# Kernel optimization log

Measured on AMD Instinct MI355X. Metric: run time of the kernel, lower is better.

The kernel has to match this reference:

```python
import jax, jax.numpy as jnp
import numpy as np

B, N, F = 32, 64, 128   # batch, nodes, input features (F == hidden_dim)
E = N * (N - 1)         # fully-connected directed edges = 4032
H, D = 4, 64            # heads, out_dim per head
ALPHA = 0.2             # leaky relu slope


def setup_inputs() -> dict:
    key = jax.random.key(0)
    ks = jax.random.split(key, 16)
    v_self = jax.random.normal(ks[0], (B, N, F), dtype=jnp.float32)
    # fully-connected one-hot sender/receiver matrices [E, N], broadcast to [B, E, N]
    pairs = np.array([(i, j) for i in range(N) for j in range(N) if i != j])
    send = np.zeros((E, N), np.float32); send[np.arange(E), pairs[:, 0]] = 1.0
    rec = np.zeros((E, N), np.float32); rec[np.arange(E), pairs[:, 1]] = 1.0
    rel_send = jnp.broadcast_to(jnp.asarray(send), (B, E, N))
    rel_rec = jnp.broadcast_to(jnp.asarray(rec), (B, E, N))
    s = 0.05
    return {
        "v_self": v_self,
        "rel_rec": rel_rec,
        "rel_send": rel_send,
        "W_proj": jax.random.normal(ks[1], (H * D, F), dtype=jnp.float32) * s,
        "a_fwd": jax.random.normal(ks[2], (H, D), dtype=jnp.float32) * s,
        "a_bwd": jax.random.normal(ks[3], (H, D), dtype=jnp.float32) * s,
        "We1": jax.random.normal(ks[4], (D, 2 * D), dtype=jnp.float32) * s,
        "be1": jnp.zeros((D,), jnp.float32),
        "We2": jax.random.normal(ks[5], (D, D), dtype=jnp.float32) * s,
        "be2": jnp.zeros((D,), jnp.float32),
        "Wv1": jax.random.normal(ks[6], (F, D), dtype=jnp.float32) * s,
        "bv1": jnp.zeros((F,), jnp.float32),
        "Wv2": jax.random.normal(ks[7], (F, F), dtype=jnp.float32) * s,
        "bv2": jnp.zeros((F,), jnp.float32),
        "Wv3": jax.random.normal(ks[8], (D, F), dtype=jnp.float32) * s,
        "bv3": jnp.zeros((D,), jnp.float32),
    }


def _leaky(x):
    return jnp.where(x >= 0, x, ALPHA * x)


def reference(v_self, rel_rec, rel_send, W_proj, a_fwd, a_bwd,
              We1, be1, We2, be2, Wv1, bv1, Wv2, bv2, Wv3, bv3):
    # project: [B,N,F] -> [B,N,H,D]
    v_proj = (v_self @ W_proj.T).reshape(B, N, H, D)
    # gather to edges via one-hot adjacency (v_src==h_src, v_tgt==h_tgt in original)
    h_src = jnp.einsum('ben,bnhd->behd', rel_send, v_proj)
    h_tgt = jnp.einsum('ben,bnhd->behd', rel_rec, v_proj)
    attn_ij = _leaky(jnp.einsum('behd,hd->beh', h_src, a_fwd)) / 500.0
    attn_ji = _leaky(jnp.einsum('behd,hd->beh', h_tgt, a_bwd)) / 500.0
    attn_max = jnp.maximum(attn_ij, attn_ji)
    # NOTE: original applies exp twice (exp of exp); reproduced faithfully
    e_ij = jnp.exp(jnp.exp(attn_ij - attn_max))
    e_ji = jnp.exp(jnp.exp(attn_ji - attn_max))
    alpha_sum = e_ij + e_ji
    alpha_ij = e_ij / alpha_sum   # [B,E,H]
    alpha_ji = e_ji / alpha_sum
    edge_input = jnp.concatenate(
        [alpha_ij[..., None] * h_src, alpha_ji[..., None] * h_tgt], axis=-1)  # [B,E,H,2D]
    # f_CG_e: Linear(2D->D), ReLU, Linear(D->D) on last dim
    e_cg = jax.nn.relu(edge_input @ We1.T + be1) @ We2.T + be2
    edge_weighted = e_cg * alpha_ij[..., None]                               # [B,E,H,D]
    # scatter back to nodes
    v_social = jnp.einsum('behd,ben->bnhd', edge_weighted, rel_rec)          # [B,N,H,D]
    # f_CG_v: Linear(D->F), ReLU, Linear(F->F), ReLU, Linear(F->D)
    x = jax.nn.relu(v_social @ Wv1.T + bv1)
    x = jax.nn.relu(x @ Wv2.T + bv2)
    x = x @ Wv3.T + bv3
    v_out = x.reshape(B, N, H * D)  # concat_heads=True
    return (v_out, alpha_ij)
```

## Files before the change

### kernel.cpp

```cpp
#include <hip/hip_runtime.h>

#define B_ 32
#define N_ 64
#define F_ 128
#define E_ 4032
#define H_ 4
#define D_ 64

typedef __bf16 bf16x8 __attribute__((ext_vector_type(8)));
typedef __bf16 bf16x4 __attribute__((ext_vector_type(4)));
typedef float  f32x4  __attribute__((ext_vector_type(4)));


static __device__ inline bf16x8 ld_cvt8(const float* __restrict__ p) {
    float4 w0 = *(const float4*)p, w1 = *(const float4*)(p + 4);
    bf16x8 b;
    b[0]=(__bf16)w0.x; b[1]=(__bf16)w0.y; b[2]=(__bf16)w0.z; b[3]=(__bf16)w0.w;
    b[4]=(__bf16)w1.x; b[5]=(__bf16)w1.y; b[6]=(__bf16)w1.z; b[7]=(__bf16)w1.w;
    return b;
}

__global__ __launch_bounds__(64) void k_proj(
    const float* __restrict__ v_self, const float* __restrict__ W_proj,
    const float* __restrict__ We1,
    const float* __restrict__ a_fwd, const float* __restrict__ a_bwd,
    const float* __restrict__ Wv1, const float* __restrict__ We2,
    const float* __restrict__ be2, const float* __restrict__ Wv2,
    const float* __restrict__ Wv3,
    float* __restrict__ s_fwd, float* __restrict__ s_bwd,
    __bf16* __restrict__ u_src, __bf16* __restrict__ u_tgt,
    __bf16* __restrict__ M1bf, float* __restrict__ wb,
    __bf16* __restrict__ Wv2bf, __bf16* __restrict__ Wv3bf)
{
    const int t = threadIdx.x;
    const int blk = blockIdx.x;

    if (blk >= 512) {
        const int f = blk - 512;
        const int k = t;
        const int pid = f * 64 + k;
        float acc = 0.f;
        for (int dd = 0; dd < 64; ++dd)
            acc += Wv1[f * 64 + dd] * We2[dd * 64 + k];
        M1bf[pid] = (__bf16)acc;
        float p = Wv1[f * 64 + k] * be2[k];
#pragma unroll
        for (int m = 1; m < 64; m <<= 1) p += __shfl_xor(p, m);
        if (k == 0) wb[f] = p;
        Wv2bf[pid]        = (__bf16)Wv2[pid];
        Wv2bf[pid + 8192] = (__bf16)Wv2[pid + 8192];
        Wv3bf[pid]        = (__bf16)Wv3[pid];
        return;
    }

    const int tile = blk >> 2, w = blk & 3;
    const int node0 = tile * 16;
    const int q = t >> 4, lr = t & 15;

    __shared__ __bf16 P_lds[16 * 72];

    f32x4 acc[4] = {};
#pragma unroll
    for (int ks = 0; ks < 4; ++ks) {
        bf16x8 a = ld_cvt8(v_self + (size_t)(node0 + lr) * 128 + ks * 32 + q * 8);
#pragma unroll
        for (int ct = 0; ct < 4; ++ct) {
            bf16x8 bb = ld_cvt8(W_proj + (size_t)(w * 64 + ct * 16 + lr) * 128 + ks * 32 + q * 8);
            acc[ct] = __builtin_amdgcn_mfma_f32_16x16x32_bf16(a, bb, acc[ct], 0, 0, 0);
        }
    }

    {
        float pf[4] = {0,0,0,0}, pb[4] = {0,0,0,0};
#pragma unroll
        for (int ct = 0; ct < 4; ++ct) {
            float af = a_fwd[w * 64 + ct * 16 + lr];
            float ab = a_bwd[w * 64 + ct * 16 + lr];
#pragma unroll
            for (int r = 0; r < 4; ++r) { pf[r] += acc[ct][r] * af; pb[r] += acc[ct][r] * ab; }
        }
#pragma unroll
        for (int m = 1; m < 16; m <<= 1) {
#pragma unroll
            for (int r = 0; r < 4; ++r) { pf[r] += __shfl_xor(pf[r], m); pb[r] += __shfl_xor(pb[r], m); }
        }
        if (lr == 0) {
#pragma unroll
            for (int r = 0; r < 4; ++r) {
                float x = pf[r]; x = (x >= 0.f ? x : 0.2f * x) * 0.002f;
                float y = pb[r]; y = (y >= 0.f ? y : 0.2f * y) * 0.002f;
                s_fwd[(node0 + q * 4 + r) * 4 + w] = x;
                s_bwd[(node0 + q * 4 + r) * 4 + w] = y;
            }
        }
    }

#pragma unroll
    for (int ct = 0; ct < 4; ++ct)
#pragma unroll
        for (int r = 0; r < 4; ++r)
            P_lds[(q * 4 + r) * 72 + ct * 16 + lr] = (__bf16)acc[ct][r];
    __syncthreads();

    f32x4 us[4] = {}, ut[4] = {};
#pragma unroll
    for (int ks = 0; ks < 2; ++ks) {
        bf16x8 a = *(const bf16x8*)&P_lds[lr * 72 + ks * 32 + q * 8];
#pragma unroll
        for (int ct = 0; ct < 4; ++ct) {
            bf16x8 bs = ld_cvt8(We1 + (size_t)(ct * 16 + lr) * 128 + ks * 32 + q * 8);
            us[ct] = __builtin_amdgcn_mfma_f32_16x16x32_bf16(a, bs, us[ct], 0, 0, 0);
            bf16x8 bt = ld_cvt8(We1 + (size_t)(ct * 16 + lr) * 128 + 64 + ks * 32 + q * 8);
            ut[ct] = __builtin_amdgcn_mfma_f32_16x16x32_bf16(a, bt, ut[ct], 0, 0, 0);
        }
    }
#pragma unroll
    for (int ct = 0; ct < 4; ++ct)
#pragma unroll
        for (int r = 0; r < 4; ++r) {
            size_t row = (size_t)(node0 + q * 4 + r) * 4 + w;
            u_src[row * 64 + ct * 16 + lr] = (__bf16)us[ct][r];
            u_tgt[row * 64 + ct * 16 + lr] = (__bf16)ut[ct][r];
        }
}

__global__ __launch_bounds__(256) void k_fused(
    const float* __restrict__ s_fwd, const float* __restrict__ s_bwd,
    const __bf16* __restrict__ u_src, const __bf16* __restrict__ u_tgt,
    const float* __restrict__ be1,
    const __bf16* __restrict__ M1bf, const float* __restrict__ wb,
    const float* __restrict__ bv1,
    const __bf16* __restrict__ Wv2bf, const float* __restrict__ bv2,
    const __bf16* __restrict__ Wv3bf, const float* __restrict__ bv3,
    float* __restrict__ v_out, float* __restrict__ out_alpha)
{
    const int t = threadIdx.x;
    const int h = t >> 6, d = t & 63;
    const int b = blockIdx.x >> 4, quad = blockIdx.x & 15;
    const int j0 = quad * 4;

    __shared__ float  ut_l[4][4][64];
    __shared__ float  aij_l[4][64][4];
    __shared__ float  suma_l[16];
    __shared__ __bf16 g_l[16 * 72];
    __shared__ __bf16 X1[16 * 136];
    __shared__ __bf16 X2[16 * 136];

    {
        int idx = t * 4;
        bf16x4 v = *(const bf16x4*)(u_tgt + (size_t)(b * 64 + j0) * 256 + idx);
        int j = idx >> 8, col = idx & 255;
        f32x4 f;
#pragma unroll
        for (int z = 0; z < 4; ++z) f[z] = (float)v[z];
        *(f32x4*)&ut_l[j][col >> 6][col & 63] = f;
    }

    {
        const int i = d;
        float sfi = s_fwd[(b * 64 + i) * 4 + h];
        float areg[4];
#pragma unroll
        for (int jl = 0; jl < 4; ++jl) {
            float sbj = s_bwd[(b * 64 + j0 + jl) * 4 + h];
            float m = fmaxf(sfi, sbj);
            float eij = __expf(__expf(sfi - m));
            float eji = __expf(__expf(sbj - m));
            float aij = eij / (eij + eji);
            if (i == j0 + jl) aij = 0.f;
            areg[jl] = aij;
        }
        f32x4 a4 = {areg[0], areg[1], areg[2], areg[3]};
        *(f32x4*)&aij_l[h][i][0] = a4;
#pragma unroll
        for (int jl = 0; jl < 4; ++jl) {
            float sa = areg[jl];
#pragma unroll
            for (int m2 = 1; m2 < 64; m2 <<= 1) sa += __shfl_xor(sa, m2);
            if (i == 0) suma_l[jl * 4 + h] = sa;
        }
    }
    if (t < 252) {
        const int jj = t >> 2, h2 = t & 3;
#pragma unroll
        for (int s = 0; s < 4; ++s) {
            int i2 = j0 + s;
            int j2 = jj + (jj >= i2 ? 1 : 0);
            float sfi = s_fwd[(b * 64 + i2) * 4 + h2];
            float sbj = s_bwd[(b * 64 + j2) * 4 + h2];
            float m = fmaxf(sfi, sbj);
            float eij = __expf(__expf(sfi - m));
            float eji = __expf(__expf(sbj - m));
            out_alpha[((size_t)b * E_ + i2 * 63 + jj) * 4 + h2] = eij / (eij + eji);
        }
    }
    __syncthreads();

    {
        const float be1d = be1[d];
        float utv[4], utb[4];
#pragma unroll
        for (int jl = 0; jl < 4; ++jl) { utv[jl] = ut_l[jl][h][d]; utb[jl] = utv[jl] + be1d; }
        float gacc[4] = {};
        const __bf16* usp = u_src + ((size_t)(b * 64) * 4 + h) * 64 + d;
#pragma unroll 4
        for (int i = 0; i < 64; ++i) {
            float usv = (float)usp[i * 256];
            f32x4 a4 = *(const f32x4*)&aij_l[h][i][0];
#pragma unroll
            for (int jl = 0; jl < 4; ++jl) {
                float a = a4[jl];
                float hp = fmaf(a, usv - utv[jl], utb[jl]);
                gacc[jl] = fmaf(a, fmaxf(hp, 0.f), gacc[jl]);
            }
        }
#pragma unroll
        for (int jl = 0; jl < 4; ++jl)
            g_l[(jl * 4 + h) * 72 + d] = (__bf16)gacc[jl];
    }
    __syncthreads();

    const int w = h;
    const int q = d >> 4, lr = d & 15;

    f32x4 acc1[2] = {};
#pragma unroll
    for (int ks = 0; ks < 2; ++ks) {
        bf16x8 a = *(const bf16x8*)&g_l[lr * 72 + ks * 32 + q * 8];
#pragma unroll
        for (int c = 0; c < 2; ++c) {
            int ct = w * 2 + c;
            bf16x8 bb = *(const bf16x8*)(M1bf + (size_t)(ct * 16 + lr) * 64 + ks * 32 + q * 8);
            acc1[c] = __builtin_amdgcn_mfma_f32_16x16x32_bf16(a, bb, acc1[c], 0, 0, 0);
        }
    }
    float sml[4];
#pragma unroll
    for (int r = 0; r < 4; ++r) sml[r] = suma_l[q * 4 + r];
#pragma unroll
    for (int c = 0; c < 2; ++c) {
        int f = (w * 2 + c) * 16 + lr;
        float wbf = wb[f], b1 = bv1[f];
#pragma unroll
        for (int r = 0; r < 4; ++r) {
            float xv = acc1[c][r] + sml[r] * wbf + b1;
            X1[(q * 4 + r) * 136 + f] = (__bf16)fmaxf(xv, 0.f);
        }
    }
    __syncthreads();

    f32x4 acc2[2] = {};
#pragma unroll
    for (int ks = 0; ks < 4; ++ks) {
        bf16x8 a = *(const bf16x8*)&X1[lr * 136 + ks * 32 + q * 8];
#pragma unroll
        for (int c = 0; c < 2; ++c) {
            int ct = w * 2 + c;
            bf16x8 bb = *(const bf16x8*)(Wv2bf + (size_t)(ct * 16 + lr) * 128 + ks * 32 + q * 8);
            acc2[c] = __builtin_amdgcn_mfma_f32_16x16x32_bf16(a, bb, acc2[c], 0, 0, 0);
        }
    }
#pragma unroll
    for (int c = 0; c < 2; ++c) {
        int f = (w * 2 + c) * 16 + lr;
        float b2 = bv2[f];
#pragma unroll
        for (int r = 0; r < 4; ++r) {
            float xv = acc2[c][r] + b2;
            X2[(q * 4 + r) * 136 + f] = (__bf16)fmaxf(xv, 0.f);
        }
    }
    __syncthreads();

    f32x4 acc3 = {};
#pragma unroll
    for (int ks = 0; ks < 4; ++ks) {
        bf16x8 a = *(const bf16x8*)&X2[lr * 136 + ks * 32 + q * 8];
        bf16x8 bb = *(const bf16x8*)(Wv3bf + (size_t)(w * 16 + lr) * 128 + ks * 32 + q * 8);
        acc3 = __builtin_amdgcn_mfma_f32_16x16x32_bf16(a, bb, acc3, 0, 0, 0);
    }
    {
        int dd = w * 16 + lr;
        float b3 = bv3[dd];
        size_t rows_base = (size_t)(b * 64 + j0) * 4;
#pragma unroll
        for (int r = 0; r < 4; ++r)
            v_out[(rows_base + q * 4 + r) * 64 + dd] = acc3[r] + b3;
    }
}

extern "C" void kernel_launch(void* const* d_in, const int* in_sizes, int n_in,
                              void* d_out, int out_size, void* d_ws, size_t ws_size,
                              hipStream_t stream) {
    (void)in_sizes; (void)n_in; (void)out_size; (void)ws_size;
    const float* v_self = (const float*)d_in[0];
    const float* W_proj = (const float*)d_in[3];
    const float* a_fwd  = (const float*)d_in[4];
    const float* a_bwd  = (const float*)d_in[5];
    const float* We1    = (const float*)d_in[6];
    const float* be1    = (const float*)d_in[7];
    const float* We2    = (const float*)d_in[8];
    const float* be2    = (const float*)d_in[9];
    const float* Wv1    = (const float*)d_in[10];
    const float* bv1    = (const float*)d_in[11];
    const float* Wv2    = (const float*)d_in[12];
    const float* bv2    = (const float*)d_in[13];
    const float* Wv3    = (const float*)d_in[14];
    const float* bv3    = (const float*)d_in[15];

    float* ws = (float*)d_ws;
    float*  s_fwd = ws;
    float*  s_bwd = ws + 8192;
    float*  wb    = ws + 24576;
    __bf16* M1bf  = (__bf16*)(ws + 24704);
    __bf16* Wv2bf = (__bf16*)(ws + 28800);
    __bf16* Wv3bf = (__bf16*)(ws + 36992);
    __bf16* u_src = (__bf16*)(ws + 61568);
    __bf16* u_tgt = (__bf16*)(ws + 323712);

    float* v_out = (float*)d_out;
    float* alpha = v_out + (size_t)B_ * N_ * H_ * D_;

    hipLaunchKernelGGL(k_proj, dim3(512 + 128), dim3(64), 0, stream,
                       v_self, W_proj, We1, a_fwd, a_bwd, Wv1, We2, be2, Wv2, Wv3,
                       s_fwd, s_bwd, u_src, u_tgt, M1bf, wb, Wv2bf, Wv3bf);
    hipLaunchKernelGGL(k_fused, dim3(B_ * N_ / 4), dim3(256), 0, stream,
                       s_fwd, s_bwd, u_src, u_tgt, be1, M1bf, wb, bv1,
                       Wv2bf, bv2, Wv3bf, bv3, v_out, alpha);
}
```

Measured before the change: 29.11 us.

## Split projection K-loop and We1 halves across waves in 256-thread blocks

k_proj now runs 256-thread blocks holding two projection tiles. The two waves of each tile split the W_proj K-loop, and their partial accumulators are summed through LDS. In the second stage each wave computes either the u_src or the u_tgt half of the We1 product. The weight-prep branch is repacked to 256 threads per block, and the k_fused edge loop unroll goes from 4 to 8. The aim is shorter per-wave serial MFMA chains and fewer launched blocks, at the cost of an extra LDS reduction and barrier.

```diff
diff --git a/kernel.cpp b/kernel.cpp
--- a/kernel.cpp
+++ b/kernel.cpp
@@ -20,7 +20,7 @@
     return b;
 }
 
-__global__ __launch_bounds__(64) void k_proj(
+__global__ __launch_bounds__(256) void k_proj(
     const float* __restrict__ v_self, const float* __restrict__ W_proj,
     const float* __restrict__ We1,
     const float* __restrict__ a_fwd, const float* __restrict__ a_bwd,
@@ -35,11 +35,11 @@
     const int t = threadIdx.x;
     const int blk = blockIdx.x;
 
-    if (blk >= 512) {
-        const int f = blk - 512;
-        const int k = t;
-        const int pid = f * 64 + k;
+    if (blk >= 256) {
+        const int pid = (blk - 256) * 256 + t;
+        const int f = pid >> 6, k = pid & 63;
         float acc = 0.f;
+#pragma unroll 8
         for (int dd = 0; dd < 64; ++dd)
             acc += Wv1[f * 64 + dd] * We2[dd * 64 + k];
         M1bf[pid] = (__bf16)acc;
@@ -53,15 +53,20 @@
         return;
     }
 
-    const int tile = blk >> 2, w = blk & 3;
+    const int u = t >> 7;
+    const int wsub = (t >> 6) & 1;
+    const int l = t & 63, q = l >> 4, lr = l & 15;
+    const int gu = blk * 2 + u;
+    const int tile = gu >> 2, w = gu & 3;
     const int node0 = tile * 16;
-    const int q = t >> 4, lr = t & 15;
-
-    __shared__ __bf16 P_lds[16 * 72];
+
+    __shared__ float  accp[2][16][68];
+    __shared__ __bf16 P_lds[2][16 * 72];
 
     f32x4 acc[4] = {};
 #pragma unroll
-    for (int ks = 0; ks < 4; ++ks) {
+    for (int kk = 0; kk < 2; ++kk) {
+        int ks = wsub * 2 + kk;
         bf16x8 a = ld_cvt8(v_self + (size_t)(node0 + lr) * 128 + ks * 32 + q * 8);
 #pragma unroll
         for (int ct = 0; ct < 4; ++ct) {
@@ -69,15 +74,28 @@
             acc[ct] = __builtin_amdgcn_mfma_f32_16x16x32_bf16(a, bb, acc[ct], 0, 0, 0);
         }
     }
-
-    {
+    if (wsub == 1) {
+#pragma unroll
+        for (int ct = 0; ct < 4; ++ct)
+#pragma unroll
+            for (int r = 0; r < 4; ++r)
+                accp[u][q * 4 + r][ct * 16 + lr] = acc[ct][r];
+    }
+    __syncthreads();
+
+    if (wsub == 0) {
         float pf[4] = {0,0,0,0}, pb[4] = {0,0,0,0};
 #pragma unroll
         for (int ct = 0; ct < 4; ++ct) {
             float af = a_fwd[w * 64 + ct * 16 + lr];
             float ab = a_bwd[w * 64 + ct * 16 + lr];
 #pragma unroll
-            for (int r = 0; r < 4; ++r) { pf[r] += acc[ct][r] * af; pb[r] += acc[ct][r] * ab; }
+            for (int r = 0; r < 4; ++r) {
+                float full = acc[ct][r] + accp[u][q * 4 + r][ct * 16 + lr];
+                acc[ct][r] = full;
+                pf[r] += full * af;
+                pb[r] += full * ab;
+            }
         }
 #pragma unroll
         for (int m = 1; m < 16; m <<= 1) {
@@ -93,34 +111,32 @@
                 s_bwd[(node0 + q * 4 + r) * 4 + w] = y;
             }
         }
-    }
-
-#pragma unroll
-    for (int ct = 0; ct < 4; ++ct)
-#pragma unroll
-        for (int r = 0; r < 4; ++r)
-            P_lds[(q * 4 + r) * 72 + ct * 16 + lr] = (__bf16)acc[ct][r];
-    __syncthreads();
-
-    f32x4 us[4] = {}, ut[4] = {};
+#pragma unroll
+        for (int ct = 0; ct < 4; ++ct)
+#pragma unroll
+            for (int r = 0; r < 4; ++r)
+                P_lds[u][(q * 4 + r) * 72 + ct * 16 + lr] = (__bf16)acc[ct][r];
+    }
+    __syncthreads();
+
+    const int mm = wsub;
+    f32x4 uacc[4] = {};
 #pragma unroll
     for (int ks = 0; ks < 2; ++ks) {
-        bf16x8 a = *(const bf16x8*)&P_lds[lr * 72 + ks * 32 + q * 8];
+        bf16x8 a = *(const bf16x8*)&P_lds[u][lr * 72 + ks * 32 + q * 8];
 #pragma unroll
         for (int ct = 0; ct < 4; ++ct) {
-            bf16x8 bs = ld_cvt8(We1 + (size_t)(ct * 16 + lr) * 128 + ks * 32 + q * 8);
-            us[ct] = __builtin_amdgcn_mfma_f32_16x16x32_bf16(a, bs, us[ct], 0, 0, 0);
-            bf16x8 bt = ld_cvt8(We1 + (size_t)(ct * 16 + lr) * 128 + 64 + ks * 32 + q * 8);
-            ut[ct] = __builtin_amdgcn_mfma_f32_16x16x32_bf16(a, bt, ut[ct], 0, 0, 0);
-        }
-    }
+            bf16x8 bb = ld_cvt8(We1 + (size_t)(ct * 16 + lr) * 128 + mm * 64 + ks * 32 + q * 8);
+            uacc[ct] = __builtin_amdgcn_mfma_f32_16x16x32_bf16(a, bb, uacc[ct], 0, 0, 0);
+        }
+    }
+    __bf16* up = (mm == 0) ? u_src : u_tgt;
 #pragma unroll
     for (int ct = 0; ct < 4; ++ct)
 #pragma unroll
         for (int r = 0; r < 4; ++r) {
             size_t row = (size_t)(node0 + q * 4 + r) * 4 + w;
-            u_src[row * 64 + ct * 16 + lr] = (__bf16)us[ct][r];
-            u_tgt[row * 64 + ct * 16 + lr] = (__bf16)ut[ct][r];
+            up[row * 64 + ct * 16 + lr] = (__bf16)uacc[ct][r];
         }
 }
 
@@ -203,7 +219,7 @@
         for (int jl = 0; jl < 4; ++jl) { utv[jl] = ut_l[jl][h][d]; utb[jl] = utv[jl] + be1d; }
         float gacc[4] = {};
         const __bf16* usp = u_src + ((size_t)(b * 64) * 4 + h) * 64 + d;
-#pragma unroll 4
+#pragma unroll 8
         for (int i = 0; i < 64; ++i) {
             float usv = (float)usp[i * 256];
             f32x4 a4 = *(const f32x4*)&aij_l[h][i][0];
@@ -321,7 +337,7 @@
     float* v_out = (float*)d_out;
     float* alpha = v_out + (size_t)B_ * N_ * H_ * D_;
 
-    hipLaunchKernelGGL(k_proj, dim3(512 + 128), dim3(64), 0, stream,
+    hipLaunchKernelGGL(k_proj, dim3(256 + 32), dim3(256), 0, stream,
                        v_self, W_proj, We1, a_fwd, a_bwd, Wv1, We2, be2, Wv2, Wv3,
                        s_fwd, s_bwd, u_src, u_tgt, M1bf, wb, Wv2bf, Wv3bf);
     hipLaunchKernelGGL(k_fused, dim3(B_ * N_ / 4), dim3(256), 0, stream,
```

New measurement: 26.14 us. 10.2% less time.

## Fuse projection and We1 GEMMs into main kernel, keep per-batch intermediates in LDS

Applied to the files above, without the earlier changes.

The projection GEMM, attention scores and u_src/u_tgt products move from the prep kernel into the main kernel. Each block recomputes the whole batch's projection (64 nodes × 4 heads) and keeps u_src, s_fwd and s_bwd in shared memory, so the global round trip for these intermediates goes away. The prep kernel now only converts inputs and weights to bf16. The cost is that each batch's projection is computed redundantly by all 16 blocks of that batch, and the main kernel uses more LDS and registers, which can lower occupancy.

```diff
diff --git a/kernel.cpp b/kernel.cpp
--- a/kernel.cpp
+++ b/kernel.cpp
@@ -8,125 +8,58 @@
 #define D_ 64
 
 typedef __bf16 bf16x8 __attribute__((ext_vector_type(8)));
-typedef __bf16 bf16x4 __attribute__((ext_vector_type(4)));
 typedef float  f32x4  __attribute__((ext_vector_type(4)));
 
 
-static __device__ inline bf16x8 ld_cvt8(const float* __restrict__ p) {
-    float4 w0 = *(const float4*)p, w1 = *(const float4*)(p + 4);
-    bf16x8 b;
-    b[0]=(__bf16)w0.x; b[1]=(__bf16)w0.y; b[2]=(__bf16)w0.z; b[3]=(__bf16)w0.w;
-    b[4]=(__bf16)w1.x; b[5]=(__bf16)w1.y; b[6]=(__bf16)w1.z; b[7]=(__bf16)w1.w;
-    return b;
-}
-
-__global__ __launch_bounds__(64) void k_proj(
+#define MFMA(a, b, c) __builtin_amdgcn_mfma_f32_16x16x32_bf16(a, b, c, 0, 0, 0)
+
+__global__ __launch_bounds__(256) void k_prep(
     const float* __restrict__ v_self, const float* __restrict__ W_proj,
-    const float* __restrict__ We1,
-    const float* __restrict__ a_fwd, const float* __restrict__ a_bwd,
-    const float* __restrict__ Wv1, const float* __restrict__ We2,
-    const float* __restrict__ be2, const float* __restrict__ Wv2,
-    const float* __restrict__ Wv3,
-    float* __restrict__ s_fwd, float* __restrict__ s_bwd,
-    __bf16* __restrict__ u_src, __bf16* __restrict__ u_tgt,
-    __bf16* __restrict__ M1bf, float* __restrict__ wb,
-    __bf16* __restrict__ Wv2bf, __bf16* __restrict__ Wv3bf)
+    const float* __restrict__ We1, const float* __restrict__ Wv1,
+    const float* __restrict__ We2, const float* __restrict__ be2,
+    const float* __restrict__ Wv2, const float* __restrict__ Wv3,
+    __bf16* __restrict__ vbf, __bf16* __restrict__ Wpbf,
+    __bf16* __restrict__ We1bf, __bf16* __restrict__ M1bf,
+    float* __restrict__ wb, __bf16* __restrict__ Wv2bf,
+    __bf16* __restrict__ Wv3bf)
 {
     const int t = threadIdx.x;
     const int blk = blockIdx.x;
 
-    if (blk >= 512) {
-        const int f = blk - 512;
-        const int k = t;
-        const int pid = f * 64 + k;
-        float acc = 0.f;
-        for (int dd = 0; dd < 64; ++dd)
-            acc += Wv1[f * 64 + dd] * We2[dd * 64 + k];
-        M1bf[pid] = (__bf16)acc;
-        float p = Wv1[f * 64 + k] * be2[k];
-#pragma unroll
-        for (int m = 1; m < 64; m <<= 1) p += __shfl_xor(p, m);
-        if (k == 0) wb[f] = p;
-        Wv2bf[pid]        = (__bf16)Wv2[pid];
-        Wv2bf[pid + 8192] = (__bf16)Wv2[pid + 8192];
-        Wv3bf[pid]        = (__bf16)Wv3[pid];
+    if (blk < 128) {
+        int idx = blk * 2048 + t * 8;
+        float4 v0 = *(const float4*)(v_self + idx);
+        float4 v1 = *(const float4*)(v_self + idx + 4);
+        bf16x8 b;
+        b[0]=(__bf16)v0.x; b[1]=(__bf16)v0.y; b[2]=(__bf16)v0.z; b[3]=(__bf16)v0.w;
+        b[4]=(__bf16)v1.x; b[5]=(__bf16)v1.y; b[6]=(__bf16)v1.z; b[7]=(__bf16)v1.w;
+        *(bf16x8*)(vbf + idx) = b;
         return;
     }
 
-    const int tile = blk >> 2, w = blk & 3;
-    const int node0 = tile * 16;
-    const int q = t >> 4, lr = t & 15;
-
-    __shared__ __bf16 P_lds[16 * 72];
-
-    f32x4 acc[4] = {};
-#pragma unroll
-    for (int ks = 0; ks < 4; ++ks) {
-        bf16x8 a = ld_cvt8(v_self + (size_t)(node0 + lr) * 128 + ks * 32 + q * 8);
-#pragma unroll
-        for (int ct = 0; ct < 4; ++ct) {
-            bf16x8 bb = ld_cvt8(W_proj + (size_t)(w * 64 + ct * 16 + lr) * 128 + ks * 32 + q * 8);
-            acc[ct] = __builtin_amdgcn_mfma_f32_16x16x32_bf16(a, bb, acc[ct], 0, 0, 0);
-        }
-    }
-
-    {
-        float pf[4] = {0,0,0,0}, pb[4] = {0,0,0,0};
-#pragma unroll
-        for (int ct = 0; ct < 4; ++ct) {
-            float af = a_fwd[w * 64 + ct * 16 + lr];
-            float ab = a_bwd[w * 64 + ct * 16 + lr];
-#pragma unroll
-            for (int r = 0; r < 4; ++r) { pf[r] += acc[ct][r] * af; pb[r] += acc[ct][r] * ab; }
-        }
-#pragma unroll
-        for (int m = 1; m < 16; m <<= 1) {
-#pragma unroll
-            for (int r = 0; r < 4; ++r) { pf[r] += __shfl_xor(pf[r], m); pb[r] += __shfl_xor(pb[r], m); }
-        }
-        if (lr == 0) {
-#pragma unroll
-            for (int r = 0; r < 4; ++r) {
-                float x = pf[r]; x = (x >= 0.f ? x : 0.2f * x) * 0.002f;
-                float y = pb[r]; y = (y >= 0.f ? y : 0.2f * y) * 0.002f;
-                s_fwd[(node0 + q * 4 + r) * 4 + w] = x;
-                s_bwd[(node0 + q * 4 + r) * 4 + w] = y;
-            }
-        }
-    }
-
-#pragma unroll
-    for (int ct = 0; ct < 4; ++ct)
-#pragma unroll
-        for (int r = 0; r < 4; ++r)
-            P_lds[(q * 4 + r) * 72 + ct * 16 + lr] = (__bf16)acc[ct][r];
-    __syncthreads();
-
-    f32x4 us[4] = {}, ut[4] = {};
-#pragma unroll
-    for (int ks = 0; ks < 2; ++ks) {
-        bf16x8 a = *(const bf16x8*)&P_lds[lr * 72 + ks * 32 + q * 8];
-#pragma unroll
-        for (int ct = 0; ct < 4; ++ct) {
-            bf16x8 bs = ld_cvt8(We1 + (size_t)(ct * 16 + lr) * 128 + ks * 32 + q * 8);
-            us[ct] = __builtin_amdgcn_mfma_f32_16x16x32_bf16(a, bs, us[ct], 0, 0, 0);
-            bf16x8 bt = ld_cvt8(We1 + (size_t)(ct * 16 + lr) * 128 + 64 + ks * 32 + q * 8);
-            ut[ct] = __builtin_amdgcn_mfma_f32_16x16x32_bf16(a, bt, ut[ct], 0, 0, 0);
-        }
-    }
-#pragma unroll
-    for (int ct = 0; ct < 4; ++ct)
-#pragma unroll
-        for (int r = 0; r < 4; ++r) {
-            size_t row = (size_t)(node0 + q * 4 + r) * 4 + w;
-            u_src[row * 64 + ct * 16 + lr] = (__bf16)us[ct][r];
-            u_tgt[row * 64 + ct * 16 + lr] = (__bf16)ut[ct][r];
-        }
+    const int pid = (blk - 128) * 256 + t;
+    const int f = pid >> 6, k = pid & 63;
+    float acc = 0.f;
+#pragma unroll 8
+    for (int dd = 0; dd < 64; ++dd)
+        acc += Wv1[f * 64 + dd] * We2[dd * 64 + k];
+    M1bf[pid] = (__bf16)acc;
+    float p = Wv1[f * 64 + k] * be2[k];
+#pragma unroll
+    for (int m = 1; m < 64; m <<= 1) p += __shfl_xor(p, m);
+    if (k == 0) wb[f] = p;
+    Wv2bf[pid]        = (__bf16)Wv2[pid];
+    Wv2bf[pid + 8192] = (__bf16)Wv2[pid + 8192];
+    Wv3bf[pid]        = (__bf16)Wv3[pid];
+#pragma unroll
+    for (int z = 0; z < 4; ++z) Wpbf[pid * 4 + z] = (__bf16)W_proj[pid * 4 + z];
+    We1bf[pid] = (__bf16)We1[((pid >> 6) & 63) * 128 + (pid >> 12) * 64 + (pid & 63)];
 }
 
-__global__ __launch_bounds__(256) void k_fused(
-    const float* __restrict__ s_fwd, const float* __restrict__ s_bwd,
-    const __bf16* __restrict__ u_src, const __bf16* __restrict__ u_tgt,
+__global__ __launch_bounds__(256, 2) void k_main(
+    const __bf16* __restrict__ vbf, const __bf16* __restrict__ Wpbf,
+    const __bf16* __restrict__ We1bf,
+    const float* __restrict__ a_fwd, const float* __restrict__ a_bwd,
     const float* __restrict__ be1,
     const __bf16* __restrict__ M1bf, const float* __restrict__ wb,
     const float* __restrict__ bv1,
@@ -135,34 +68,122 @@
     float* __restrict__ v_out, float* __restrict__ out_alpha)
 {
     const int t = threadIdx.x;
-    const int h = t >> 6, d = t & 63;
+    const int h = t >> 6;
+    const int l = t & 63, q = l >> 4, lr = l & 15;
     const int b = blockIdx.x >> 4, quad = blockIdx.x & 15;
     const int j0 = quad * 4;
 
+    __shared__ __bf16 u_src_l[4][64][64];
+    __shared__ __bf16 P_l[4][64][72];
+    __shared__ float  s_fwd_l[4][64], s_bwd_l[4][64];
     __shared__ float  ut_l[4][4][64];
     __shared__ float  aij_l[4][64][4];
     __shared__ float  suma_l[16];
-    __shared__ __bf16 g_l[16 * 72];
-    __shared__ __bf16 X1[16 * 136];
-    __shared__ __bf16 X2[16 * 136];
+
+    __bf16* g_l = &P_l[0][0][0];
+    __bf16* X1  = g_l + 16 * 72;
+    __bf16* X2  = X1 + 16 * 136;
+
+    f32x4 acc[4][4] = {};
+#pragma unroll
+    for (int ks = 0; ks < 4; ++ks) {
+        bf16x8 av[4];
+#pragma unroll
+        for (int nt = 0; nt < 4; ++nt)
+            av[nt] = *(const bf16x8*)(vbf + (size_t)(b * 64 + nt * 16 + lr) * 128 + ks * 32 + q * 8);
+#pragma unroll
+        for (int ct = 0; ct < 4; ++ct) {
+            bf16x8 bb = *(const bf16x8*)(Wpbf + (size_t)(h * 64 + ct * 16 + lr) * 128 + ks * 32 + q * 8);
+#pragma unroll
+            for (int nt = 0; nt < 4; ++nt)
+                acc[nt][ct] = MFMA(av[nt], bb, acc[nt][ct]);
+        }
+    }
 
     {
-        int idx = t * 4;
-        bf16x4 v = *(const bf16x4*)(u_tgt + (size_t)(b * 64 + j0) * 256 + idx);
-        int j = idx >> 8, col = idx & 255;
-        f32x4 f;
-#pragma unroll
-        for (int z = 0; z < 4; ++z) f[z] = (float)v[z];
-        *(f32x4*)&ut_l[j][col >> 6][col & 63] = f;
+        float af[4], ab[4];
+#pragma unroll
+        for (int ct = 0; ct < 4; ++ct) {
+            af[ct] = a_fwd[h * 64 + ct * 16 + lr];
+            ab[ct] = a_bwd[h * 64 + ct * 16 + lr];
+        }
+#pragma unroll
+        for (int nt = 0; nt < 4; ++nt) {
+            float pf[4] = {0,0,0,0}, pb[4] = {0,0,0,0};
+#pragma unroll
+            for (int ct = 0; ct < 4; ++ct)
+#pragma unroll
+                for (int r = 0; r < 4; ++r) {
+                    pf[r] += acc[nt][ct][r] * af[ct];
+                    pb[r] += acc[nt][ct][r] * ab[ct];
+                }
+#pragma unroll
+            for (int m = 1; m < 16; m <<= 1)
+#pragma unroll
+                for (int r = 0; r < 4; ++r) { pf[r] += __shfl_xor(pf[r], m); pb[r] += __shfl_xor(pb[r], m); }
+            if (lr == 0) {
+#pragma unroll
+                for (int r = 0; r < 4; ++r) {
+                    int node = nt * 16 + q * 4 + r;
+                    float x = pf[r]; x = (x >= 0.f ? x : 0.2f * x) * 0.002f;
+                    float y = pb[r]; y = (y >= 0.f ? y : 0.2f * y) * 0.002f;
+                    s_fwd_l[h][node] = x;
+                    s_bwd_l[h][node] = y;
+                }
+            }
+#pragma unroll
+            for (int ct = 0; ct < 4; ++ct)
+#pragma unroll
+                for (int r = 0; r < 4; ++r)
+                    P_l[h][nt * 16 + q * 4 + r][ct * 16 + lr] = (__bf16)acc[nt][ct][r];
+        }
+    }
+    __syncthreads();
+
+#pragma unroll
+    for (int half = 0; half < 2; ++half) {
+        f32x4 uacc[4][4] = {};
+#pragma unroll
+        for (int ks = 0; ks < 2; ++ks) {
+            bf16x8 a[4];
+#pragma unroll
+            for (int rt = 0; rt < 4; ++rt)
+                a[rt] = *(const bf16x8*)&P_l[h][rt * 16 + lr][ks * 32 + q * 8];
+#pragma unroll
+            for (int ct = 0; ct < 4; ++ct) {
+                bf16x8 bb = *(const bf16x8*)(We1bf + (size_t)(half * 64 + ct * 16 + lr) * 64 + ks * 32 + q * 8);
+#pragma unroll
+                for (int rt = 0; rt < 4; ++rt)
+                    uacc[rt][ct] = MFMA(a[rt], bb, uacc[rt][ct]);
+            }
+        }
+        if (half == 0) {
+#pragma unroll
+            for (int rt = 0; rt < 4; ++rt)
+#pragma unroll
+                for (int ct = 0; ct < 4; ++ct)
+#pragma unroll
+                    for (int r = 0; r < 4; ++r)
+                        u_src_l[h][rt * 16 + q * 4 + r][ct * 16 + lr] = (__bf16)uacc[rt][ct][r];
+        } else {
+            const int rtq = quad >> 2;
+            if (q == (quad & 3)) {
+#pragma unroll
+                for (int ct = 0; ct < 4; ++ct)
+#pragma unroll
+                    for (int r = 0; r < 4; ++r)
+                        ut_l[r][h][ct * 16 + lr] = uacc[rtq][ct][r];
+            }
+        }
     }
 
     {
-        const int i = d;
-        float sfi = s_fwd[(b * 64 + i) * 4 + h];
+        const int i = l;
+        float sfi = s_fwd_l[h][i];
         float areg[4];
 #pragma unroll
         for (int jl = 0; jl < 4; ++jl) {
-            float sbj = s_bwd[(b * 64 + j0 + jl) * 4 + h];
+            float sbj = s_bwd_l[h][j0 + jl];
             float m = fmaxf(sfi, sbj);
             float eij = __expf(__expf(sfi - m));
             float eji = __expf(__expf(sbj - m));
@@ -186,8 +207,8 @@
         for (int s = 0; s < 4; ++s) {
             int i2 = j0 + s;
             int j2 = jj + (jj >= i2 ? 1 : 0);
-            float sfi = s_fwd[(b * 64 + i2) * 4 + h2];
-            float sbj = s_bwd[(b * 64 + j2) * 4 + h2];
+            float sfi = s_fwd_l[h2][i2];
+            float sbj = s_bwd_l[h2][j2];
             float m = fmaxf(sfi, sbj);
             float eij = __expf(__expf(sfi - m));
             float eji = __expf(__expf(sbj - m));
@@ -197,15 +218,16 @@
     __syncthreads();
 
     {
+        const int d = l;
         const float be1d = be1[d];
         float utv[4], utb[4];
 #pragma unroll
         for (int jl = 0; jl < 4; ++jl) { utv[jl] = ut_l[jl][h][d]; utb[jl] = utv[jl] + be1d; }
         float gacc[4] = {};
-        const __bf16* usp = u_src + ((size_t)(b * 64) * 4 + h) * 64 + d;
-#pragma unroll 4
+        const __bf16* usp = &u_src_l[h][0][d];
+#pragma unroll 8
         for (int i = 0; i < 64; ++i) {
-            float usv = (float)usp[i * 256];
+            float usv = (float)usp[i * 64];
             f32x4 a4 = *(const f32x4*)&aij_l[h][i][0];
 #pragma unroll
             for (int jl = 0; jl < 4; ++jl) {
@@ -216,12 +238,9 @@
         }
 #pragma unroll
         for (int jl = 0; jl < 4; ++jl)
-            g_l[(jl * 4 + h) * 72 + d] = (__bf16)gacc[jl];
-    }
-    __syncthreads();
-
-    const int w = h;
-    const int q = d >> 4, lr = d & 15;
+            g_l[(jl * 4 + h) * 72 + l] = (__bf16)gacc[jl];
+    }
+    __syncthreads();
 
     f32x4 acc1[2] = {};
 #pragma unroll
@@ -229,9 +248,9 @@
         bf16x8 a = *(const bf16x8*)&g_l[lr * 72 + ks * 32 + q * 8];
 #pragma unroll
         for (int c = 0; c < 2; ++c) {
-            int ct = w * 2 + c;
+            int ct = h * 2 + c;
             bf16x8 bb = *(const bf16x8*)(M1bf + (size_t)(ct * 16 + lr) * 64 + ks * 32 + q * 8);
-            acc1[c] = __builtin_amdgcn_mfma_f32_16x16x32_bf16(a, bb, acc1[c], 0, 0, 0);
+            acc1[c] = MFMA(a, bb, acc1[c]);
         }
     }
     float sml[4];
@@ -239,7 +258,7 @@
     for (int r = 0; r < 4; ++r) sml[r] = suma_l[q * 4 + r];
 #pragma unroll
     for (int c = 0; c < 2; ++c) {
-        int f = (w * 2 + c) * 16 + lr;
+        int f = (h * 2 + c) * 16 + lr;
         float wbf = wb[f], b1 = bv1[f];
 #pragma unroll
         for (int r = 0; r < 4; ++r) {
@@ -255,14 +274,14 @@
         bf16x8 a = *(const bf16x8*)&X1[lr * 136 + ks * 32 + q * 8];
 #pragma unroll
         for (int c = 0; c < 2; ++c) {
-            int ct = w * 2 + c;
+            int ct = h * 2 + c;
             bf16x8 bb = *(const bf16x8*)(Wv2bf + (size_t)(ct * 16 + lr) * 128 + ks * 32 + q * 8);
-            acc2[c] = __builtin_amdgcn_mfma_f32_16x16x32_bf16(a, bb, acc2[c], 0, 0, 0);
+            acc2[c] = MFMA(a, bb, acc2[c]);
         }
     }
 #pragma unroll
     for (int c = 0; c < 2; ++c) {
-        int f = (w * 2 + c) * 16 + lr;
+        int f = (h * 2 + c) * 16 + lr;
         float b2 = bv2[f];
 #pragma unroll
         for (int r = 0; r < 4; ++r) {
@@ -276,11 +295,11 @@
 #pragma unroll
     for (int ks = 0; ks < 4; ++ks) {
         bf16x8 a = *(const bf16x8*)&X2[lr * 136 + ks * 32 + q * 8];
-        bf16x8 bb = *(const bf16x8*)(Wv3bf + (size_t)(w * 16 + lr) * 128 + ks * 32 + q * 8);
-        acc3 = __builtin_amdgcn_mfma_f32_16x16x32_bf16(a, bb, acc3, 0, 0, 0);
+        bf16x8 bb = *(const bf16x8*)(Wv3bf + (size_t)(h * 16 + lr) * 128 + ks * 32 + q * 8);
+        acc3 = MFMA(a, bb, acc3);
     }
     {
-        int dd = w * 16 + lr;
+        int dd = h * 16 + lr;
         float b3 = bv3[dd];
         size_t rows_base = (size_t)(b * 64 + j0) * 4;
 #pragma unroll
@@ -309,22 +328,21 @@
     const float* bv3    = (const float*)d_in[15];
 
     float* ws = (float*)d_ws;
-    float*  s_fwd = ws;
-    float*  s_bwd = ws + 8192;
     float*  wb    = ws + 24576;
     __bf16* M1bf  = (__bf16*)(ws + 24704);
     __bf16* Wv2bf = (__bf16*)(ws + 28800);
     __bf16* Wv3bf = (__bf16*)(ws + 36992);
-    __bf16* u_src = (__bf16*)(ws + 61568);
-    __bf16* u_tgt = (__bf16*)(ws + 323712);
+    __bf16* Wpbf  = (__bf16*)(ws + 41088);
+    __bf16* We1bf = (__bf16*)(ws + 57472);
+    __bf16* vbf   = (__bf16*)(ws + 61568);
 
     float* v_out = (float*)d_out;
     float* alpha = v_out + (size_t)B_ * N_ * H_ * D_;
 
-    hipLaunchKernelGGL(k_proj, dim3(512 + 128), dim3(64), 0, stream,
-                       v_self, W_proj, We1, a_fwd, a_bwd, Wv1, We2, be2, Wv2, Wv3,
-                       s_fwd, s_bwd, u_src, u_tgt, M1bf, wb, Wv2bf, Wv3bf);
-    hipLaunchKernelGGL(k_fused, dim3(B_ * N_ / 4), dim3(256), 0, stream,
-                       s_fwd, s_bwd, u_src, u_tgt, be1, M1bf, wb, bv1,
+    hipLaunchKernelGGL(k_prep, dim3(160), dim3(256), 0, stream,
+                       v_self, W_proj, We1, Wv1, We2, be2, Wv2, Wv3,
+                       vbf, Wpbf, We1bf, M1bf, wb, Wv2bf, Wv3bf);
+    hipLaunchKernelGGL(k_main, dim3(B_ * N_ / 4), dim3(256), 0, stream,
+                       vbf, Wpbf, We1bf, a_fwd, a_bwd, be1, M1bf, wb, bv1,
                        Wv2bf, bv2, Wv3bf, bv3, v_out, alpha);
 }
```

New measurement: 40.69 us. 39.8% more time.

## Split projection across four waves per block and stage u_src in LDS

Applied to the files above, without the earlier changes.

k_proj now runs 256 threads per block. Each wave computes one 16-column tile of the projection. The attention-logit partial sums are reduced across waves through LDS, and the We1 products are split between waves by source/target half and column pair. The weight-prep blocks are remapped to 32 blocks of 256 threads. k_fused bulk-copies the batch's u_src slice (32 KB bf16) into LDS with vectorized coalesced loads, so the 64-iteration edge reduction reads from LDS rather than doing strided global loads. This trades extra LDS per block, and possibly lower occupancy, for shorter per-wave dependency chains and cheaper reduction reads.

```diff
diff --git a/kernel.cpp b/kernel.cpp
--- a/kernel.cpp
+++ b/kernel.cpp
@@ -10,6 +10,8 @@
 typedef __bf16 bf16x8 __attribute__((ext_vector_type(8)));
 typedef __bf16 bf16x4 __attribute__((ext_vector_type(4)));
 typedef float  f32x4  __attribute__((ext_vector_type(4)));
+
+#define MFMA(a, b, c) __builtin_amdgcn_mfma_f32_16x16x32_bf16(a, b, c, 0, 0, 0)
 
 
 static __device__ inline bf16x8 ld_cvt8(const float* __restrict__ p) {
@@ -20,7 +22,7 @@
     return b;
 }
 
-__global__ __launch_bounds__(64) void k_proj(
+__global__ __launch_bounds__(256) void k_proj(
     const float* __restrict__ v_self, const float* __restrict__ W_proj,
     const float* __restrict__ We1,
     const float* __restrict__ a_fwd, const float* __restrict__ a_bwd,
@@ -35,11 +37,11 @@
     const int t = threadIdx.x;
     const int blk = blockIdx.x;
 
-    if (blk >= 512) {
-        const int f = blk - 512;
-        const int k = t;
-        const int pid = f * 64 + k;
+    if (blk < 32) {
+        const int pid = blk * 256 + t;
+        const int f = pid >> 6, k = pid & 63;
         float acc = 0.f;
+#pragma unroll 8
         for (int dd = 0; dd < 64; ++dd)
             acc += Wv1[f * 64 + dd] * We2[dd * 64 + k];
         M1bf[pid] = (__bf16)acc;
@@ -53,74 +55,74 @@
         return;
     }
 
-    const int tile = blk >> 2, w = blk & 3;
+    const int bid = blk - 32;
+    const int tile = bid >> 2, w = bid & 3;
     const int node0 = tile * 16;
-    const int q = t >> 4, lr = t & 15;
+    const int wsub = t >> 6;
+    const int l = t & 63, q = l >> 4, lr = l & 15;
 
     __shared__ __bf16 P_lds[16 * 72];
-
-    f32x4 acc[4] = {};
+    __shared__ float  spart_f[4][16], spart_b[4][16];
+
+    f32x4 acc = {};
 #pragma unroll
     for (int ks = 0; ks < 4; ++ks) {
         bf16x8 a = ld_cvt8(v_self + (size_t)(node0 + lr) * 128 + ks * 32 + q * 8);
-#pragma unroll
-        for (int ct = 0; ct < 4; ++ct) {
-            bf16x8 bb = ld_cvt8(W_proj + (size_t)(w * 64 + ct * 16 + lr) * 128 + ks * 32 + q * 8);
-            acc[ct] = __builtin_amdgcn_mfma_f32_16x16x32_bf16(a, bb, acc[ct], 0, 0, 0);
-        }
-    }
-
-    {
-        float pf[4] = {0,0,0,0}, pb[4] = {0,0,0,0};
-#pragma unroll
-        for (int ct = 0; ct < 4; ++ct) {
-            float af = a_fwd[w * 64 + ct * 16 + lr];
-            float ab = a_bwd[w * 64 + ct * 16 + lr];
-#pragma unroll
-            for (int r = 0; r < 4; ++r) { pf[r] += acc[ct][r] * af; pb[r] += acc[ct][r] * ab; }
-        }
-#pragma unroll
-        for (int m = 1; m < 16; m <<= 1) {
+        bf16x8 bb = ld_cvt8(W_proj + (size_t)(w * 64 + wsub * 16 + lr) * 128 + ks * 32 + q * 8);
+        acc = MFMA(a, bb, acc);
+    }
+
+    {
+        float af = a_fwd[w * 64 + wsub * 16 + lr];
+        float ab = a_bwd[w * 64 + wsub * 16 + lr];
+        float pf[4], pb[4];
+#pragma unroll
+        for (int r = 0; r < 4; ++r) { pf[r] = acc[r] * af; pb[r] = acc[r] * ab; }
+#pragma unroll
+        for (int m = 1; m < 16; m <<= 1)
 #pragma unroll
             for (int r = 0; r < 4; ++r) { pf[r] += __shfl_xor(pf[r], m); pb[r] += __shfl_xor(pb[r], m); }
-        }
         if (lr == 0) {
 #pragma unroll
             for (int r = 0; r < 4; ++r) {
-                float x = pf[r]; x = (x >= 0.f ? x : 0.2f * x) * 0.002f;
-                float y = pb[r]; y = (y >= 0.f ? y : 0.2f * y) * 0.002f;
-                s_fwd[(node0 + q * 4 + r) * 4 + w] = x;
-                s_bwd[(node0 + q * 4 + r) * 4 + w] = y;
+                spart_f[wsub][q * 4 + r] = pf[r];
+                spart_b[wsub][q * 4 + r] = pb[r];
             }
         }
-    }
-
-#pragma unroll
-    for (int ct = 0; ct < 4; ++ct)
 #pragma unroll
         for (int r = 0; r < 4; ++r)
-            P_lds[(q * 4 + r) * 72 + ct * 16 + lr] = (__bf16)acc[ct][r];
-    __syncthreads();
-
-    f32x4 us[4] = {}, ut[4] = {};
+            P_lds[(q * 4 + r) * 72 + wsub * 16 + lr] = (__bf16)acc[r];
+    }
+    __syncthreads();
+
+    if (t < 16) {
+        float sf = spart_f[0][t] + spart_f[1][t] + spart_f[2][t] + spart_f[3][t];
+        float sb = spart_b[0][t] + spart_b[1][t] + spart_b[2][t] + spart_b[3][t];
+        sf = (sf >= 0.f ? sf : 0.2f * sf) * 0.002f;
+        sb = (sb >= 0.f ? sb : 0.2f * sb) * 0.002f;
+        s_fwd[(node0 + t) * 4 + w] = sf;
+        s_bwd[(node0 + t) * 4 + w] = sb;
+    }
+
+    const int mm = wsub >> 1, cp = wsub & 1;
+    f32x4 uacc[2] = {};
 #pragma unroll
     for (int ks = 0; ks < 2; ++ks) {
         bf16x8 a = *(const bf16x8*)&P_lds[lr * 72 + ks * 32 + q * 8];
 #pragma unroll
-        for (int ct = 0; ct < 4; ++ct) {
-            bf16x8 bs = ld_cvt8(We1 + (size_t)(ct * 16 + lr) * 128 + ks * 32 + q * 8);
-            us[ct] = __builtin_amdgcn_mfma_f32_16x16x32_bf16(a, bs, us[ct], 0, 0, 0);
-            bf16x8 bt = ld_cvt8(We1 + (size_t)(ct * 16 + lr) * 128 + 64 + ks * 32 + q * 8);
-            ut[ct] = __builtin_amdgcn_mfma_f32_16x16x32_bf16(a, bt, ut[ct], 0, 0, 0);
-        }
-    }
-#pragma unroll
-    for (int ct = 0; ct < 4; ++ct)
+        for (int c = 0; c < 2; ++c) {
+            int ct = cp * 2 + c;
+            bf16x8 bb = ld_cvt8(We1 + (size_t)(ct * 16 + lr) * 128 + mm * 64 + ks * 32 + q * 8);
+            uacc[c] = MFMA(a, bb, uacc[c]);
+        }
+    }
+    __bf16* up = (mm == 0) ? u_src : u_tgt;
+#pragma unroll
+    for (int c = 0; c < 2; ++c)
 #pragma unroll
         for (int r = 0; r < 4; ++r) {
             size_t row = (size_t)(node0 + q * 4 + r) * 4 + w;
-            u_src[row * 64 + ct * 16 + lr] = (__bf16)us[ct][r];
-            u_tgt[row * 64 + ct * 16 + lr] = (__bf16)ut[ct][r];
+            up[row * 64 + (cp * 2 + c) * 16 + lr] = (__bf16)uacc[c][r];
         }
 }
 
@@ -139,6 +141,7 @@
     const int b = blockIdx.x >> 4, quad = blockIdx.x & 15;
     const int j0 = quad * 4;
 
+    __shared__ __bf16 us_l[64][4][64];
     __shared__ float  ut_l[4][4][64];
     __shared__ float  aij_l[4][64][4];
     __shared__ float  suma_l[16];
@@ -146,6 +149,15 @@
     __shared__ __bf16 X1[16 * 136];
     __shared__ __bf16 X2[16 * 136];
 
+    {
+        const __bf16* ub = u_src + (size_t)b * 16384;
+        __bf16* dst = &us_l[0][0][0];
+#pragma unroll
+        for (int it = 0; it < 8; ++it) {
+            int idx = it * 2048 + t * 8;
+            *(bf16x8*)(dst + idx) = *(const bf16x8*)(ub + idx);
+        }
+    }
     {
         int idx = t * 4;
         bf16x4 v = *(const bf16x4*)(u_tgt + (size_t)(b * 64 + j0) * 256 + idx);
@@ -202,8 +214,8 @@
 #pragma unroll
         for (int jl = 0; jl < 4; ++jl) { utv[jl] = ut_l[jl][h][d]; utb[jl] = utv[jl] + be1d; }
         float gacc[4] = {};
-        const __bf16* usp = u_src + ((size_t)(b * 64) * 4 + h) * 64 + d;
-#pragma unroll 4
+        const __bf16* usp = &us_l[0][h][d];
+#pragma unroll 8
         for (int i = 0; i < 64; ++i) {
             float usv = (float)usp[i * 256];
             f32x4 a4 = *(const f32x4*)&aij_l[h][i][0];
@@ -231,7 +243,7 @@
         for (int c = 0; c < 2; ++c) {
             int ct = w * 2 + c;
             bf16x8 bb = *(const bf16x8*)(M1bf + (size_t)(ct * 16 + lr) * 64 + ks * 32 + q * 8);
-            acc1[c] = __builtin_amdgcn_mfma_f32_16x16x32_bf16(a, bb, acc1[c], 0, 0, 0);
+            acc1[c] = MFMA(a, bb, acc1[c]);
         }
     }
     float sml[4];
@@ -257,7 +269,7 @@
         for (int c = 0; c < 2; ++c) {
             int ct = w * 2 + c;
             bf16x8 bb = *(const bf16x8*)(Wv2bf + (size_t)(ct * 16 + lr) * 128 + ks * 32 + q * 8);
-            acc2[c] = __builtin_amdgcn_mfma_f32_16x16x32_bf16(a, bb, acc2[c], 0, 0, 0);
+            acc2[c] = MFMA(a, bb, acc2[c]);
         }
     }
 #pragma unroll
@@ -277,7 +289,7 @@
     for (int ks = 0; ks < 4; ++ks) {
         bf16x8 a = *(const bf16x8*)&X2[lr * 136 + ks * 32 + q * 8];
         bf16x8 bb = *(const bf16x8*)(Wv3bf + (size_t)(w * 16 + lr) * 128 + ks * 32 + q * 8);
-        acc3 = __builtin_amdgcn_mfma_f32_16x16x32_bf16(a, bb, acc3, 0, 0, 0);
+        acc3 = MFMA(a, bb, acc3);
     }
     {
         int dd = w * 16 + lr;
@@ -321,7 +333,7 @@
     float* v_out = (float*)d_out;
     float* alpha = v_out + (size_t)B_ * N_ * H_ * D_;
 
-    hipLaunchKernelGGL(k_proj, dim3(512 + 128), dim3(64), 0, stream,
+    hipLaunchKernelGGL(k_proj, dim3(32 + 512), dim3(256), 0, stream,
                        v_self, W_proj, We1, a_fwd, a_bwd, Wv1, We2, be2, Wv2, Wv3,
                        s_fwd, s_bwd, u_src, u_tgt, M1bf, wb, Wv2bf, Wv3bf);
     hipLaunchKernelGGL(k_fused, dim3(B_ * N_ / 4), dim3(256), 0, stream,
```

New measurement: 26.53 us. 1.1x faster.
